# Kernel optimization log

Measured on AMD Instinct MI355X. Metric: run time of the kernel, lower is better.

## Reference

```python
import jax, jax.numpy as jnp
import numpy as np


def setup_inputs() -> dict:
    key = jax.random.key(0)
    B, T, D = 16, 2048, 256
    inputs = jax.random.normal(key, (B, T, D), dtype=jnp.float32)
    return {"inputs": inputs, "window_size": 7}


def reference(inputs, window_size):
    # Faithful to the keras layer: output[b, t] = concat(x[t], x[t-1], ..., x[t-W+1])
    # with zeros where t-k < 0. Built with one pad + W shifted views instead of
    # the original O(W^2) pad/concat loop.
    B, T, D = inputs.shape
    W = window_size
    padded = jnp.pad(inputs, ((0, 0), (W - 1, 0), (0, 0)))  # [B, T+W-1, D]
    # slice k gives x shifted right by k (i.e., x[t-k]) over the valid range
    pieces = [padded[:, W - 1 - k : W - 1 - k + T, :] for k in range(W)]
    return jnp.concatenate(pieces, axis=2)  # [B, T, W*D]
```

## Files before the change

kernel.cpp:

```cpp
#include <hip/hip_runtime.h>
#include <hip/hip_bf16.h>


typedef float vf4 __attribute__((ext_vector_type(4)));

constexpr int B  = 16;
constexpr int T  = 2048;
constexpr int D  = 256;
constexpr int W  = 7;
constexpr int D4 = D / 4;
constexpr int ROW4 = W * D4;
constexpr int CHUNK = 4;
constexpr int TOTAL4 = B * T * D4;
constexpr int S = TOTAL4 / CHUNK;
constexpr int SROW = S / D4;
constexpr int SOUT = SROW * ROW4;

__global__ __launch_bounds__(256) void window_scatter4_plain_kernel(
    const vf4* __restrict__ in, vf4* __restrict__ out) {
  int i0  = blockIdx.x * 256 + threadIdx.x;
  int row = i0 >> 6;
  int dd  = i0 & 63;
  int t   = row & (T - 1);

  vf4 v[CHUNK];
#pragma unroll
  for (int c = 0; c < CHUNK; ++c)
    v[c] = in[i0 + c * S];

  int base = row * ROW4 + dd;

#pragma unroll
  for (int w = 0; w < W; ++w) {
    if (t + w < T) {
#pragma unroll
      for (int c = 0; c < CHUNK; ++c)
        out[base + c * SOUT + w * (ROW4 + D4)] = v[c];
    }
  }

  if (t < W - 1) {
    vf4 z = {0.f, 0.f, 0.f, 0.f};
    for (int w = t + 1; w < W; ++w) {
#pragma unroll
      for (int c = 0; c < CHUNK; ++c)
        out[base + c * SOUT + w * D4] = z;
    }
  }
}

extern "C" void kernel_launch(void* const* d_in, const int* in_sizes, int n_in,
                              void* d_out, int out_size, void* d_ws, size_t ws_size,
                              hipStream_t stream) {
  const vf4* in = (const vf4*)d_in[0];
  vf4* out = (vf4*)d_out;
  window_scatter4_plain_kernel<<<S / 256, 256, 0, stream>>>(in, out);
}
```

Baseline: 253.9 us.

## Replace scatter-style window copy with per-block gather over contiguous output rows

Switches from a scatter formulation, where each thread reads one input vector and writes it to up to seven output positions spread across rows, to a gather formulation. Each block now owns 16 consecutive output rows and its 448 threads write full contiguous output rows, each thread reading the input row shifted by its window offset. Zero padding is handled in the branch for the first block of each sequence. The output write stream becomes fully sequential per block, at the cost of input rows being re-read by several window lanes, which should mostly hit in cache.

```diff
diff --git a/kernel.cpp b/kernel.cpp
--- a/kernel.cpp
+++ b/kernel.cpp
@@ -1,51 +1,46 @@
 #include <hip/hip_runtime.h>
-#include <hip/hip_bf16.h>
 
 
 typedef float vf4 __attribute__((ext_vector_type(4)));
 
-constexpr int B  = 16;
-constexpr int T  = 2048;
-constexpr int D  = 256;
-constexpr int W  = 7;
-constexpr int D4 = D / 4;
+constexpr int B    = 16;
+constexpr int T    = 2048;
+constexpr int D    = 256;
+constexpr int W    = 7;
+constexpr int D4   = D / 4;
 constexpr int ROW4 = W * D4;
-constexpr int CHUNK = 4;
-constexpr int TOTAL4 = B * T * D4;
-constexpr int S = TOTAL4 / CHUNK;
-constexpr int SROW = S / D4;
-constexpr int SOUT = SROW * ROW4;
+constexpr int RPB  = 16;
+constexpr int NROW = B * T;
+constexpr int NBLK = NROW / RPB;
 
-__global__ __launch_bounds__(256) void window_scatter4_plain_kernel(
+__global__ __launch_bounds__(W * 64) void window_gather_kernel(
     const vf4* __restrict__ in, vf4* __restrict__ out) {
-  int i0  = blockIdx.x * 256 + threadIdx.x;
-  int row = i0 >> 6;
-  int dd  = i0 & 63;
-  int t   = row & (T - 1);
+  const int w  = threadIdx.x >> 6;
+  const int dd = threadIdx.x & 63;
+  const int r0 = blockIdx.x * RPB;
+  const int t0 = r0 & (T - 1);
 
-  vf4 v[CHUNK];
+  vf4* dst = out + (size_t)r0 * ROW4 + w * D4 + dd;
+
+  if (t0 != 0) {
+    const vf4* src = in + (r0 - w) * D4 + dd;
+    vf4 v[RPB];
 #pragma unroll
-  for (int c = 0; c < CHUNK; ++c)
-    v[c] = in[i0 + c * S];
-
-  int base = row * ROW4 + dd;
-
+    for (int i = 0; i < RPB; ++i) v[i] = src[i * D4];
 #pragma unroll
-  for (int w = 0; w < W; ++w) {
-    if (t + w < T) {
+    for (int i = 0; i < RPB; ++i) dst[i * ROW4] = v[i];
+  } else {
+    vf4 v[RPB];
 #pragma unroll
-      for (int c = 0; c < CHUNK; ++c)
-        out[base + c * SOUT + w * (ROW4 + D4)] = v[c];
+    for (int i = 0; i < RPB; ++i) {
+      int sr = r0 + i - w;
+      if (sr < 0) sr = 0;
+      vf4 ld = in[sr * D4 + dd];
+      vf4 z  = {0.f, 0.f, 0.f, 0.f};
+      v[i] = (i >= w) ? ld : z;
     }
-  }
-
-  if (t < W - 1) {
-    vf4 z = {0.f, 0.f, 0.f, 0.f};
-    for (int w = t + 1; w < W; ++w) {
 #pragma unroll
-      for (int c = 0; c < CHUNK; ++c)
-        out[base + c * SOUT + w * D4] = z;
-    }
+    for (int i = 0; i < RPB; ++i) dst[i * ROW4] = v[i];
   }
 }
 
@@ -54,5 +49,5 @@
                               hipStream_t stream) {
   const vf4* in = (const vf4*)d_in[0];
   vf4* out = (vf4*)d_out;
-  window_scatter4_plain_kernel<<<S / 256, 256, 0, stream>>>(in, out);
+  window_gather_kernel<<<NBLK, W * 64, 0, stream>>>(in, out);
 }
```

Result: slower. 259.8 us (+2.3%).
